# Performance work log

Measured on AMD Instinct MI355X. Metric: run time of the kernel, lower is better.

Reference implementation:

```python
import jax, jax.numpy as jnp
import numpy as np


def setup_inputs() -> dict:
    key = jax.random.key(0)
    x = jax.random.normal(key, (8, 4096, 512), dtype=jnp.float32)
    kappa = jnp.float32(0.5)
    return {"x": x, "kappa": kappa}


def reference(x, kappa):
    # Faithful reduction of DecorrLoss.forward (batched=False path).
    # Original math per flattened sample n (N = B*L samples, feature dim d):
    #   D_n = diag(x_n^2); V_n = D_n - I; C_n = x_n x_n^T - D_n
    #   corr = mean_n mean_{ij} C_n^2
    #   whit = mean_n mean_{ij} V_n^2
    #   grad = mean_n [(1-kappa)*C_n + kappa*V_n]
    # Algebraic identities avoid the O(N*d^2) intermediate:
    #   mean_{ij} C_n^2 = ((sum_i x_i^2)^2 - sum_i x_i^4) / d^2   (off-diag outer products)
    #   mean_{ij} V_n^2 = sum_i (x_i^2 - 1)^2 / d^2               (V is diagonal)
    #   mean_n C_n = X^T X / N with diagonal zeroed
    #   mean_n V_n = diag(mean_n x^2 - 1)
    b, l, d = x.shape
    xf = x.reshape(b * l, d)          # (N, d)
    n = xf.shape[0]
    x2 = xf * xf                      # (N, d)

    s2 = jnp.sum(x2, axis=1)          # (N,) sum of squares per sample
    s4 = jnp.sum(x2 * x2, axis=1)     # (N,) sum of fourth powers per sample
    inv_d2 = 1.0 / (d * d)
    correlation_loss = jnp.mean(s2 * s2 - s4) * inv_d2
    whitening_loss = jnp.mean(jnp.sum((x2 - 1.0) ** 2, axis=1)) * inv_d2

    gram = (xf.T @ xf) / n            # (d, d) = mean_n x_n x_n^T
    m2 = jnp.diagonal(gram)           # mean_n x_i^2
    off_diag = gram - jnp.diag(m2)    # mean_n C_n
    grad = (1.0 - kappa) * off_diag + kappa * jnp.diag(m2 - 1.0)
    return grad, correlation_loss, whitening_loss
```

## Files before the change

### kernel.cpp

```cpp
#include <hip/hip_runtime.h>
#include <hip/hip_bf16.h>
#include <stdint.h>


#define D 512
#define NSAMP 32768
#define KPARTS 64
#define NTILES 10
#define NCHUNK 8
#define PREP_BLOCKS 1024
#define KPARTS_FB 32
#define KC_FB 1024
#define BK_FB 64
#define NCHUNK_FB 16

typedef __bf16 bf16x8 __attribute__((ext_vector_type(8)));
typedef float floatx4 __attribute__((ext_vector_type(4)));
typedef unsigned short ushort8 __attribute__((ext_vector_type(8)));
typedef __attribute__((address_space(1))) const uint32_t gas_u32;
typedef __attribute__((address_space(3))) uint32_t las_u32;

__global__ __launch_bounds__(1024) void zero_kernel(float* out, int n) {
    int i = blockIdx.x * 1024 + threadIdx.x;
    if (i < n) out[i] = 0.0f;
}


__global__ __launch_bounds__(256) void prep_kernel(const float* __restrict__ x,
                                                   uint16_t* __restrict__ xt,
                                                   float2* __restrict__ lpart) {
    __shared__ char lds[512 * 64];
    __shared__ float sA[4], sB[4];
    const int t = threadIdx.x;
    const int l = t & 63;
    const int w = t >> 6;
    const int bb = blockIdx.x;
    const int kc = bb >> 1;
    const int h = bb & 1;
    char* xtb = (char*)xt;

    const float* base = x + ((size_t)(32 * bb + 8 * w)) * D;
    float4 va[16];
#pragma unroll
    for (int r = 0; r < 8; ++r) {
        va[2 * r]     = *(const float4*)(base + (size_t)r * D + 4 * l);
        va[2 * r + 1] = *(const float4*)(base + (size_t)r * D + 256 + 4 * l);
    }

    float p2[8], p4[8];
#pragma unroll
    for (int r = 0; r < 8; ++r) {
        float a2 = 0.f, a4 = 0.f, e;
#pragma unroll
        for (int c = 0; c < 8; ++c) {
            const float v = ((const float*)&va[2 * r])[c];
            e = v * v;
            a2 += e;
            a4 += e * e;
        }
        p2[r] = a2;
        p4[r] = a4;
    }
#pragma unroll
    for (int m = 1; m < 64; m <<= 1) {
#pragma unroll
        for (int r = 0; r < 8; ++r) {
            p2[r] += __shfl_xor(p2[r], m);
            p4[r] += __shfl_xor(p4[r], m);
        }
    }
    float accA = 0.f, accB = 0.f;
#pragma unroll
    for (int r = 0; r < 8; ++r) {
        accA += p2[r] * p2[r] - p4[r];
        accB += p4[r] - 2.0f * p2[r];
    }

    ushort8 pk[8];
#pragma unroll
    for (int c2 = 0; c2 < 8; ++c2)
#pragma unroll
        for (int r = 0; r < 8; ++r)
            pk[c2][r] = __bfloat16_as_ushort(
                __float2bfloat16(((const float*)&va[2 * r + (c2 >> 2)])[c2 & 3]));

    const int pos_w = (w ^ (l & 3)) * 16;
#pragma unroll
    for (int c2 = 0; c2 < 8; ++c2) {
        const int f = (c2 < 4) ? (4 * l + c2) : (256 + 4 * l + (c2 - 4));
        *(ushort8*)(lds + f * 64 + pos_w) = pk[c2];
    }

    if (l == 0) { sA[w] = accA; sB[w] = accB; }
    __syncthreads();
    if (t == 0) {
        lpart[bb] = make_float2(sA[0] + sA[1] + sA[2] + sA[3],
                                sB[0] + sB[1] + sB[2] + sB[3]);
    }

    const int g = l & 3;
    const int g2 = h * 4 + g;
#pragma unroll
    for (int i = 0; i < 8; ++i) {
        const int f = i * 64 + w * 16 + (l >> 2);
        const int pos_r = (g ^ (l >> 4)) * 16;
        const ushort8 v = *(const ushort8*)(lds + f * 64 + pos_r);
        const size_t addr = (size_t)f * 65536 + (size_t)kc * 128 +
                            (size_t)(((g2 ^ (f & 7)) * 16));
        *(ushort8*)(xtb + addr) = v;
    }
}

__global__ __launch_bounds__(256, 2) void gram_tri_kernel(const uint16_t* __restrict__ xt,
                                                          uint16_t* __restrict__ parts) {
    __shared__ __bf16 As[2][128 * 64];
    __shared__ __bf16 Bs[2][128 * 64];

    const int b = blockIdx.x;
    const int xcd = b & 7;
    const int s = b >> 3;
    const int kpart = xcd + 8 * (s / NTILES);
    const int tl = s % NTILES;
    const int ti = (tl < 4) ? 0 : (tl < 7) ? 1 : (tl < 9) ? 2 : 3;
    const int tj = (tl < 4) ? tl : (tl < 7) ? (tl - 3) : (tl < 9) ? (tl - 5) : 3;
    const int i0 = ti * 128;
    const int j0 = tj * 128;
    const bool diag = (ti == tj);

    const int t = threadIdx.x;
    const int l = t & 63;
    const int wv = t >> 6;
    const char* xb = (const char*)xt;

    const int frow = wv * 32 + (l >> 3);
    const size_t ga = (size_t)(i0 + frow) * 65536 + (size_t)((l & 7) * 16);
    const size_t gb = (size_t)(j0 + frow) * 65536 + (size_t)((l & 7) * 16);

    floatx4 acc[4][4];
#pragma unroll
    for (int a = 0; a < 4; ++a)
#pragma unroll
        for (int b2 = 0; b2 < 4; ++b2) acc[a][b2] = (floatx4)0.0f;

    const int wm = (wv >> 1) * 64;
    const int wn = (wv & 1) * 64;
    const int rl = l & 15;
    const int q = l >> 4;

#define STAGE(c, buf)                                                                         \
    {                                                                                         \
        const size_t koff = (size_t)(kpart * NCHUNK + (c)) * 128;                             \
        _Pragma("unroll") for (int i = 0; i < 4; ++i) {                                       \
            __builtin_amdgcn_global_load_lds((gas_u32*)(xb + ga + (size_t)i * 8 * 65536 + koff), \
                                             (las_u32*)&As[buf][(wv * 32 + i * 8) * 64], 16, 0, 0); \
        }                                                                                     \
        if (!diag) {                                                                          \
            _Pragma("unroll") for (int i = 0; i < 4; ++i) {                                   \
                __builtin_amdgcn_global_load_lds((gas_u32*)(xb + gb + (size_t)i * 8 * 65536 + koff), \
                                                 (las_u32*)&Bs[buf][(wv * 32 + i * 8) * 64], 16, 0, 0); \
            }                                                                                 \
        }                                                                                     \
    }

    STAGE(0, 0);
    for (int c = 0; c < NCHUNK; ++c) {
        __syncthreads();
        if (c + 1 < NCHUNK) STAGE(c + 1, (c + 1) & 1);
        const char* Ab = (const char*)As[c & 1];
        const char* Bb = diag ? Ab : (const char*)Bs[c & 1];
#pragma unroll
        for (int kk = 0; kk < 2; ++kk) {
            const int qp = kk * 4 + q;
            bf16x8 af[4], bfr[4];
#pragma unroll
            for (int tm = 0; tm < 4; ++tm) {
                const int fi = wm + tm * 16 + rl;
                af[tm] = *(const bf16x8*)(Ab + fi * 128 + ((qp ^ (fi & 7)) * 16));
            }
#pragma unroll
            for (int tn = 0; tn < 4; ++tn) {
                const int fj = wn + tn * 16 + rl;
                bfr[tn] = *(const bf16x8*)(Bb + fj * 128 + ((qp ^ (fj & 7)) * 16));
            }
#pragma unroll
            for (int tm = 0; tm < 4; ++tm)
#pragma unroll
                for (int tn = 0; tn < 4; ++tn)
                    acc[tm][tn] = __builtin_amdgcn_mfma_f32_16x16x32_bf16(
                        af[tm], bfr[tn], acc[tm][tn], 0, 0, 0);
        }
    }
#undef STAGE

    uint16_t* p = parts + ((size_t)kpart * NTILES + tl) * 16384;
#pragma unroll
    for (int tm = 0; tm < 4; ++tm)
#pragma unroll
        for (int tn = 0; tn < 4; ++tn)
#pragma unroll
            for (int rr = 0; rr < 4; ++rr) {
                const int gi = wm + tm * 16 + q * 4 + rr;
                const int gj = wn + tn * 16 + rl;
                p[gi * 128 + gj] = __bfloat16_as_ushort(__float2bfloat16(acc[tm][tn][rr]));
            }
}

__global__ __launch_bounds__(256) void finalize_tri_kernel(const uint16_t* __restrict__ parts,
                                                           const float2* __restrict__ lpart,
                                                           const float* __restrict__ kappa_p,
                                                           float* __restrict__ out) {
    if (blockIdx.x == 160) {
        __shared__ float sA[4], sB[4];
        const int w = threadIdx.x >> 6;
        const int l = threadIdx.x & 63;
        float a = 0.f, b = 0.f;
        for (int i = threadIdx.x; i < PREP_BLOCKS; i += 256) {
            const float2 pp = lpart[i];
            a += pp.x;
            b += pp.y;
        }
#pragma unroll
        for (int m = 1; m < 64; m <<= 1) {
            a += __shfl_xor(a, m);
            b += __shfl_xor(b, m);
        }
        if (l == 0) { sA[w] = a; sB[w] = b; }
        __syncthreads();
        if (threadIdx.x == 0) {
            const float SCALE = 1.1641532182693481e-10f;
            out[D * D] = (sA[0] + sA[1] + sA[2] + sA[3]) * SCALE;
            out[D * D + 1] = (sB[0] + sB[1] + sB[2] + sB[3]) * SCALE + 0.001953125f;
        }
        return;
    }
    const int tl = blockIdx.x / 16;
    const int strip = blockIdx.x % 16;
    const int ti = (tl < 4) ? 0 : (tl < 7) ? 1 : (tl < 9) ? 2 : 3;
    const int tj = (tl < 4) ? tl : (tl < 7) ? (tl - 3) : (tl < 9) ? (tl - 5) : 3;

    const int tr = threadIdx.x >> 5;
    const int col0 = (threadIdx.x & 31) * 4;
    const int r = strip * 8 + tr;

    float s0 = 0.f, s1 = 0.f, s2 = 0.f, s3 = 0.f;
    const uint16_t* base = parts + (size_t)tl * 16384 + r * 128 + col0;
    for (int kp = 0; kp < KPARTS; ++kp) {
        const ushort4 v = *(const ushort4*)(base + (size_t)kp * (NTILES * 16384));
        s0 += __uint_as_float((uint32_t)v.x << 16);
        s1 += __uint_as_float((uint32_t)v.y << 16);
        s2 += __uint_as_float((uint32_t)v.z << 16);
        s3 += __uint_as_float((uint32_t)v.w << 16);
    }
    const float kappa = *kappa_p;
    const float invn = 1.0f / (float)NSAMP;
    const int gi = ti * 128 + r;
    const int gj0 = tj * 128 + col0;
    float rr[4] = {s0, s1, s2, s3};
#pragma unroll
    for (int c = 0; c < 4; ++c) {
        const float m = rr[c] * invn;
        rr[c] = (gi == gj0 + c) ? kappa * (m - 1.0f) : (1.0f - kappa) * m;
    }
    float4 o = {rr[0], rr[1], rr[2], rr[3]};
    *(float4*)(out + (size_t)gi * D + gj0) = o;
    if (ti != tj) {
#pragma unroll
        for (int c = 0; c < 4; ++c) out[(size_t)(gj0 + c) * D + gi] = rr[c];
    }
}


__global__ __launch_bounds__(256) void loss_atomic_kernel(const float* __restrict__ x,
                                                          float* __restrict__ out) {
    __shared__ float sA[4], sB[4];
    const int w = threadIdx.x >> 6;
    const int l = threadIdx.x & 63;
    const int gw = blockIdx.x * 4 + w;
    const float* base = x + (size_t)gw * 4 * D;
    float4 v[8];
#pragma unroll
    for (int r = 0; r < 4; ++r) {
        v[2 * r]     = *(const float4*)(base + (size_t)r * D + l * 4);
        v[2 * r + 1] = *(const float4*)(base + (size_t)r * D + 256 + l * 4);
    }
    float p2[4], p4[4];
#pragma unroll
    for (int r = 0; r < 4; ++r) {
        const float* f = (const float*)&v[2 * r];
        float a2 = 0.f, a4 = 0.f, e;
#pragma unroll
        for (int c = 0; c < 8; ++c) { e = f[c] * f[c]; a2 += e; a4 += e * e; }
        p2[r] = a2; p4[r] = a4;
    }
#pragma unroll
    for (int m = 1; m < 64; m <<= 1) {
#pragma unroll
        for (int r = 0; r < 4; ++r) {
            p2[r] += __shfl_xor(p2[r], m);
            p4[r] += __shfl_xor(p4[r], m);
        }
    }
    float accA = 0.f, accB = 0.f;
#pragma unroll
    for (int r = 0; r < 4; ++r) {
        accA += p2[r] * p2[r] - p4[r];
        accB += p4[r] - 2.0f * p2[r];
    }
    if (l == 0) { sA[w] = accA; sB[w] = accB; }
    __syncthreads();
    if (threadIdx.x == 0) {
        const float SCALE = 1.1641532182693481e-10f;
        atomicAdd(out + D * D, (sA[0] + sA[1] + sA[2] + sA[3]) * SCALE);
        atomicAdd(out + D * D + 1, (sB[0] + sB[1] + sB[2] + sB[3]) * SCALE);
        if (blockIdx.x == 0) atomicAdd(out + D * D + 1, 0.001953125f);
    }
}

__global__ __launch_bounds__(256, 2) void gram_fp32_atomic_kernel(const float* __restrict__ x,
                                                                  float* __restrict__ dst) {
    __shared__ __bf16 As[128 * 64];
    __shared__ __bf16 Bs[128 * 64];
    char* Asb = (char*)As;
    char* Bsb = (char*)Bs;
    const int kpart = blockIdx.x & (KPARTS_FB - 1);
    const int tile = blockIdx.x >> 5;
    const int i0 = (tile & 3) * 128;
    const int j0 = (tile >> 2) * 128;
    const int kbase = kpart * KC_FB;
    const int t = threadIdx.x;
    const int l = t & 63;
    const int wv = t >> 6;
    const int fq = (l & 7) + 8 * wv;
    const int ksl = l >> 3;
    const float4* x4 = (const float4*)x;
    const int aoff = (i0 >> 2) + fq;
    const int boff = (j0 >> 2) + fq;
    float4 va[8], vb[8];
#pragma unroll
    for (int r = 0; r < 4; ++r) {
        const size_t row = (size_t)(kbase + 2 * ksl + 16 * r) * 128;
        va[2 * r] = x4[row + aoff];     va[2 * r + 1] = x4[row + 128 + aoff];
        vb[2 * r] = x4[row + boff];     vb[2 * r + 1] = x4[row + 128 + boff];
    }
    floatx4 acc[4][4];
#pragma unroll
    for (int a = 0; a < 4; ++a)
#pragma unroll
        for (int b = 0; b < 4; ++b) acc[a][b] = (floatx4)0.0f;
    const int wm = (wv >> 1) * 64;
    const int wn = (wv & 1) * 64;
    const int rl = l & 15;
    const int q = l >> 4;
    for (int c = 0; c < NCHUNK_FB; ++c) {
        __syncthreads();
#pragma unroll
        for (int r = 0; r < 4; ++r) {
            const int k0 = 2 * ksl + 16 * r;
            const int g = k0 >> 3;
            const int sb = (k0 & 7) * 2;
            const float* fa0 = (const float*)&va[2 * r];
            const float* fa1 = (const float*)&va[2 * r + 1];
            const float* fb0 = (const float*)&vb[2 * r];
            const float* fb1 = (const float*)&vb[2 * r + 1];
#pragma unroll
            for (int cc = 0; cc < 4; ++cc) {
                const int f = fq * 4 + cc;
                const int off = f * 128 + ((g ^ (f & 7)) * 16) + sb;
                unsigned int pa = (unsigned int)__bfloat16_as_ushort(__float2bfloat16(fa0[cc])) |
                                  ((unsigned int)__bfloat16_as_ushort(__float2bfloat16(fa1[cc])) << 16);
                unsigned int pb = (unsigned int)__bfloat16_as_ushort(__float2bfloat16(fb0[cc])) |
                                  ((unsigned int)__bfloat16_as_ushort(__float2bfloat16(fb1[cc])) << 16);
                *(unsigned int*)(Asb + off) = pa;
                *(unsigned int*)(Bsb + off) = pb;
            }
        }
        if (c + 1 < NCHUNK_FB) {
            const int kb = kbase + (c + 1) * BK_FB;
#pragma unroll
            for (int r = 0; r < 4; ++r) {
                const size_t row = (size_t)(kb + 2 * ksl + 16 * r) * 128;
                va[2 * r] = x4[row + aoff];     va[2 * r + 1] = x4[row + 128 + aoff];
                vb[2 * r] = x4[row + boff];     vb[2 * r + 1] = x4[row + 128 + boff];
            }
        }
        __syncthreads();
#pragma unroll
        for (int kk = 0; kk < 2; ++kk) {
            const int qp = kk * 4 + q;
            bf16x8 af[4], bfr[4];
#pragma unroll
            for (int tm = 0; tm < 4; ++tm) {
                const int fi = wm + tm * 16 + rl;
                af[tm] = *(const bf16x8*)(Asb + fi * 128 + ((qp ^ (fi & 7)) * 16));
            }
#pragma unroll
            for (int tn = 0; tn < 4; ++tn) {
                const int fj = wn + tn * 16 + rl;
                bfr[tn] = *(const bf16x8*)(Bsb + fj * 128 + ((qp ^ (fj & 7)) * 16));
            }
#pragma unroll
            for (int tm = 0; tm < 4; ++tm)
#pragma unroll
                for (int tn = 0; tn < 4; ++tn)
                    acc[tm][tn] = __builtin_amdgcn_mfma_f32_16x16x32_bf16(
                        af[tm], bfr[tn], acc[tm][tn], 0, 0, 0);
        }
    }
#pragma unroll
    for (int tm = 0; tm < 4; ++tm)
#pragma unroll
        for (int tn = 0; tn < 4; ++tn)
#pragma unroll
            for (int rr = 0; rr < 4; ++rr) {
                const int gi = i0 + wm + tm * 16 + q * 4 + rr;
                const int gj = j0 + wn + tn * 16 + rl;
                atomicAdd(dst + (size_t)gi * D + gj, acc[tm][tn][rr]);
            }
}

__global__ __launch_bounds__(256) void finalize1_kernel(const float* __restrict__ src,
                                                        const float* __restrict__ kappa_p,
                                                        float* __restrict__ out) {
    const int base = (blockIdx.x * 256 + threadIdx.x) * 4;
    float4 s = *(const float4*)(src + base);
    const float kappa = *kappa_p;
    const float invn = 1.0f / (float)NSAMP;
    const int i = base >> 9;
    const int j = base & (D - 1);
    float r[4] = {s.x, s.y, s.z, s.w};
#pragma unroll
    for (int cpt = 0; cpt < 4; ++cpt) {
        const float m = r[cpt] * invn;
        r[cpt] = (i == j + cpt) ? kappa * (m - 1.0f) : (1.0f - kappa) * m;
    }
    float4 o = {r[0], r[1], r[2], r[3]};
    *(float4*)(out + base) = o;
}

extern "C" void kernel_launch(void* const* d_in, const int* in_sizes, int n_in,
                              void* d_out, int out_size, void* d_ws, size_t ws_size,
                              hipStream_t stream) {
    const float* x = (const float*)d_in[0];
    const float* kappa = (const float*)d_in[1];
    float* out = (float*)d_out;

    const size_t xt_bytes = (size_t)D * NSAMP * sizeof(uint16_t);
    const size_t parts_bytes = (size_t)KPARTS * NTILES * 16384 * sizeof(uint16_t);
    const size_t lpart_bytes = (size_t)PREP_BLOCKS * sizeof(float2);

    if (ws_size >= xt_bytes + parts_bytes + lpart_bytes) {
        uint16_t* xt = (uint16_t*)d_ws;
        uint16_t* parts = (uint16_t*)((char*)d_ws + xt_bytes);
        float2* lpart = (float2*)((char*)d_ws + xt_bytes + parts_bytes);
        prep_kernel<<<PREP_BLOCKS, 256, 0, stream>>>(x, xt, lpart);
        gram_tri_kernel<<<8 * NTILES * (KPARTS / 8), 256, 0, stream>>>(xt, parts);
        finalize_tri_kernel<<<161, 256, 0, stream>>>(parts, lpart, kappa, out);
    } else {
        zero_kernel<<<(out_size + 1023) / 1024, 1024, 0, stream>>>(out, out_size);
        loss_atomic_kernel<<<2048, 256, 0, stream>>>(x, out);
        gram_fp32_atomic_kernel<<<16 * KPARTS_FB, 256, 0, stream>>>(x, out);
        finalize1_kernel<<<(D * D / 4) / 256, 256, 0, stream>>>(out, kappa, out);
    }
}
```

Baseline: 123.2 us.

## Switch Gram transpose buffer and MFMA from bf16 to fp8

The prep kernel now packs x into fp8 (e4m3) instead of bf16, which halves the transposed workspace and the LDS staging. The Gram kernel loads 8-byte fp8 fragments and uses the 16x16x32 fp8 MFMA, and occupancy is raised to 3 blocks per SM. This cuts global traffic for writing and reading the transposed copy. In exchange, precision drops sharply: fp8 has about 3 mantissa bits, so gram accuracy may exceed tolerance.

```diff
diff --git a/kernel.cpp b/kernel.cpp
--- a/kernel.cpp
+++ b/kernel.cpp
@@ -16,7 +16,6 @@
 
 typedef __bf16 bf16x8 __attribute__((ext_vector_type(8)));
 typedef float floatx4 __attribute__((ext_vector_type(4)));
-typedef unsigned short ushort8 __attribute__((ext_vector_type(8)));
 typedef __attribute__((address_space(1))) const uint32_t gas_u32;
 typedef __attribute__((address_space(3))) uint32_t las_u32;
 
@@ -27,9 +26,9 @@
 
 
 __global__ __launch_bounds__(256) void prep_kernel(const float* __restrict__ x,
-                                                   uint16_t* __restrict__ xt,
+                                                   uint8_t* __restrict__ xt,
                                                    float2* __restrict__ lpart) {
-    __shared__ char lds[512 * 64];
+    __shared__ char lds[512 * 32];
     __shared__ float sA[4], sB[4];
     const int t = threadIdx.x;
     const int l = t & 63;
@@ -76,19 +75,22 @@
         accB += p4[r] - 2.0f * p2[r];
     }
 
-    ushort8 pk[8];
-#pragma unroll
-    for (int c2 = 0; c2 < 8; ++c2)
+    const int pos_w = (w ^ (l & 3)) * 8;
+#pragma unroll
+    for (int c2 = 0; c2 < 8; ++c2) {
+        float s[8];
 #pragma unroll
         for (int r = 0; r < 8; ++r)
-            pk[c2][r] = __bfloat16_as_ushort(
-                __float2bfloat16(((const float*)&va[2 * r + (c2 >> 2)])[c2 & 3]));
-
-    const int pos_w = (w ^ (l & 3)) * 16;
-#pragma unroll
-    for (int c2 = 0; c2 < 8; ++c2) {
+            s[r] = ((const float*)&va[2 * r + (c2 >> 2)])[c2 & 3];
+        uint32_t w0 = __builtin_amdgcn_cvt_pk_fp8_f32(s[0], s[1], 0, false);
+        w0 = __builtin_amdgcn_cvt_pk_fp8_f32(s[2], s[3], w0, true);
+        uint32_t w1 = __builtin_amdgcn_cvt_pk_fp8_f32(s[4], s[5], 0, false);
+        w1 = __builtin_amdgcn_cvt_pk_fp8_f32(s[6], s[7], w1, true);
         const int f = (c2 < 4) ? (4 * l + c2) : (256 + 4 * l + (c2 - 4));
-        *(ushort8*)(lds + f * 64 + pos_w) = pk[c2];
+        uint2 v;
+        v.x = w0;
+        v.y = w1;
+        *(uint2*)(lds + f * 32 + pos_w) = v;
     }
 
     if (l == 0) { sA[w] = accA; sB[w] = accB; }
@@ -98,23 +100,21 @@
                                 sB[0] + sB[1] + sB[2] + sB[3]);
     }
 
-    const int g = l & 3;
-    const int g2 = h * 4 + g;
+    const int d = l & 3;
+    const int pos_r = (d ^ ((l >> 4) & 3)) * 8;
 #pragma unroll
     for (int i = 0; i < 8; ++i) {
         const int f = i * 64 + w * 16 + (l >> 2);
-        const int pos_r = (g ^ (l >> 4)) * 16;
-        const ushort8 v = *(const ushort8*)(lds + f * 64 + pos_r);
-        const size_t addr = (size_t)f * 65536 + (size_t)kc * 128 +
-                            (size_t)(((g2 ^ (f & 7)) * 16));
-        *(ushort8*)(xtb + addr) = v;
-    }
-}
-
-__global__ __launch_bounds__(256, 2) void gram_tri_kernel(const uint16_t* __restrict__ xt,
+        const uint2 v = *(const uint2*)(lds + f * 32 + pos_r);
+        const int posg = (4 * h + d) ^ (f & 7);
+        *(uint2*)(xtb + (size_t)f * 32768 + (size_t)kc * 64 + posg * 8) = v;
+    }
+}
+
+__global__ __launch_bounds__(256, 3) void gram_tri_kernel(const uint8_t* __restrict__ xt,
                                                           uint16_t* __restrict__ parts) {
-    __shared__ __bf16 As[2][128 * 64];
-    __shared__ __bf16 Bs[2][128 * 64];
+    __shared__ char As[2][128 * 64];
+    __shared__ char Bs[2][128 * 64];
 
     const int b = blockIdx.x;
     const int xcd = b & 7;
@@ -132,9 +132,9 @@
     const int wv = t >> 6;
     const char* xb = (const char*)xt;
 
-    const int frow = wv * 32 + (l >> 3);
-    const size_t ga = (size_t)(i0 + frow) * 65536 + (size_t)((l & 7) * 16);
-    const size_t gb = (size_t)(j0 + frow) * 65536 + (size_t)((l & 7) * 16);
+    const size_t lane_off = (size_t)(l >> 2) * 32768 + (size_t)((l & 3) * 16);
+    const size_t ga = (size_t)(i0 + wv * 32) * 32768 + lane_off;
+    const size_t gb = (size_t)(j0 + wv * 32) * 32768 + lane_off;
 
     floatx4 acc[4][4];
 #pragma unroll
@@ -149,15 +149,15 @@
 
 #define STAGE(c, buf)                                                                         \
     {                                                                                         \
-        const size_t koff = (size_t)(kpart * NCHUNK + (c)) * 128;                             \
-        _Pragma("unroll") for (int i = 0; i < 4; ++i) {                                       \
-            __builtin_amdgcn_global_load_lds((gas_u32*)(xb + ga + (size_t)i * 8 * 65536 + koff), \
-                                             (las_u32*)&As[buf][(wv * 32 + i * 8) * 64], 16, 0, 0); \
+        const size_t koff = (size_t)(kpart * NCHUNK + (c)) * 64;                              \
+        _Pragma("unroll") for (int i = 0; i < 2; ++i) {                                       \
+            __builtin_amdgcn_global_load_lds((gas_u32*)(xb + ga + (size_t)i * 16 * 32768 + koff), \
+                                             (las_u32*)(As[buf] + (wv * 32 + i * 16) * 64), 16, 0, 0); \
         }                                                                                     \
         if (!diag) {                                                                          \
-            _Pragma("unroll") for (int i = 0; i < 4; ++i) {                                   \
-                __builtin_amdgcn_global_load_lds((gas_u32*)(xb + gb + (size_t)i * 8 * 65536 + koff), \
-                                                 (las_u32*)&Bs[buf][(wv * 32 + i * 8) * 64], 16, 0, 0); \
+            _Pragma("unroll") for (int i = 0; i < 2; ++i) {                                   \
+                __builtin_amdgcn_global_load_lds((gas_u32*)(xb + gb + (size_t)i * 16 * 32768 + koff), \
+                                                 (las_u32*)(Bs[buf] + (wv * 32 + i * 16) * 64), 16, 0, 0); \
             }                                                                                 \
         }                                                                                     \
     }
@@ -166,27 +166,27 @@
     for (int c = 0; c < NCHUNK; ++c) {
         __syncthreads();
         if (c + 1 < NCHUNK) STAGE(c + 1, (c + 1) & 1);
-        const char* Ab = (const char*)As[c & 1];
-        const char* Bb = diag ? Ab : (const char*)Bs[c & 1];
+        const char* Ab = As[c & 1];
+        const char* Bb = diag ? Ab : Bs[c & 1];
 #pragma unroll
         for (int kk = 0; kk < 2; ++kk) {
             const int qp = kk * 4 + q;
-            bf16x8 af[4], bfr[4];
+            long af[4], bfr[4];
 #pragma unroll
             for (int tm = 0; tm < 4; ++tm) {
                 const int fi = wm + tm * 16 + rl;
-                af[tm] = *(const bf16x8*)(Ab + fi * 128 + ((qp ^ (fi & 7)) * 16));
+                af[tm] = *(const long*)(Ab + fi * 64 + ((qp ^ (fi & 7)) * 8));
             }
 #pragma unroll
             for (int tn = 0; tn < 4; ++tn) {
                 const int fj = wn + tn * 16 + rl;
-                bfr[tn] = *(const bf16x8*)(Bb + fj * 128 + ((qp ^ (fj & 7)) * 16));
+                bfr[tn] = *(const long*)(Bb + fj * 64 + ((qp ^ (fj & 7)) * 8));
             }
 #pragma unroll
             for (int tm = 0; tm < 4; ++tm)
 #pragma unroll
                 for (int tn = 0; tn < 4; ++tn)
-                    acc[tm][tn] = __builtin_amdgcn_mfma_f32_16x16x32_bf16(
+                    acc[tm][tn] = __builtin_amdgcn_mfma_f32_16x16x32_fp8_fp8(
                         af[tm], bfr[tn], acc[tm][tn], 0, 0, 0);
         }
     }
@@ -316,6 +316,7 @@
     }
 }
 
+typedef bf16x8 bf16x8_t;
 __global__ __launch_bounds__(256, 2) void gram_fp32_atomic_kernel(const float* __restrict__ x,
                                                                   float* __restrict__ dst) {
     __shared__ __bf16 As[128 * 64];
@@ -387,16 +388,16 @@
 #pragma unroll
         for (int kk = 0; kk < 2; ++kk) {
             const int qp = kk * 4 + q;
-            bf16x8 af[4], bfr[4];
+            bf16x8_t af[4], bfr[4];
 #pragma unroll
             for (int tm = 0; tm < 4; ++tm) {
                 const int fi = wm + tm * 16 + rl;
-                af[tm] = *(const bf16x8*)(Asb + fi * 128 + ((qp ^ (fi & 7)) * 16));
+                af[tm] = *(const bf16x8_t*)(Asb + fi * 128 + ((qp ^ (fi & 7)) * 16));
             }
 #pragma unroll
             for (int tn = 0; tn < 4; ++tn) {
                 const int fj = wn + tn * 16 + rl;
-                bfr[tn] = *(const bf16x8*)(Bsb + fj * 128 + ((qp ^ (fj & 7)) * 16));
+                bfr[tn] = *(const bf16x8_t*)(Bsb + fj * 128 + ((qp ^ (fj & 7)) * 16));
             }
 #pragma unroll
             for (int tm = 0; tm < 4; ++tm)
@@ -444,12 +445,12 @@
     const float* kappa = (const float*)d_in[1];
     float* out = (float*)d_out;
 
-    const size_t xt_bytes = (size_t)D * NSAMP * sizeof(uint16_t);
+    const size_t xt_bytes = (size_t)D * NSAMP;
     const size_t parts_bytes = (size_t)KPARTS * NTILES * 16384 * sizeof(uint16_t);
     const size_t lpart_bytes = (size_t)PREP_BLOCKS * sizeof(float2);
 
     if (ws_size >= xt_bytes + parts_bytes + lpart_bytes) {
-        uint16_t* xt = (uint16_t*)d_ws;
+        uint8_t* xt = (uint8_t*)d_ws;
         uint16_t* parts = (uint16_t*)((char*)d_ws + xt_bytes);
         float2* lpart = (float2*)((char*)d_ws + xt_bytes + parts_bytes);
         prep_kernel<<<PREP_BLOCKS, 256, 0, stream>>>(x, xt, lpart);
```

New measurement: 122.8 us. Within noise of the previous version (-0.3%).
